# Kernel tuning notes

Measured on AMD Instinct MI355X. Metric: run time of the kernel, lower is better.

## Reference

```python
import jax, jax.numpy as jnp
import numpy as np

N_NODES = 100000
N_EDGES = 1600000
HIDDEN = 128
N_GRAPHS = 64
N_CLASSES = 10


def setup_inputs() -> dict:
    key = jax.random.key(0)
    ks = jax.random.split(key, 10)
    x = jax.random.normal(ks[0], (N_NODES, 1), dtype=jnp.float32)
    edge_index = jax.random.randint(ks[1], (2, N_EDGES), 0, N_NODES, dtype=jnp.int32)
    batch = jnp.sort(jax.random.randint(ks[2], (N_NODES,), 0, N_GRAPHS, dtype=jnp.int32))
    def glorot(k, shape):
        fan_in, fan_out = shape
        s = jnp.sqrt(6.0 / (fan_in + fan_out))
        return jax.random.uniform(k, shape, jnp.float32, -s, s)
    return {
        "x": x,
        "edge_index": edge_index,
        "batch": batch,
        "W1l": glorot(ks[3], (1, HIDDEN)),
        "W1r": glorot(ks[4], (1, HIDDEN)),
        "b1": jnp.zeros((HIDDEN,), jnp.float32),
        "W2l": glorot(ks[5], (HIDDEN, HIDDEN)),
        "W2r": glorot(ks[6], (HIDDEN, HIDDEN)),
        "b2": jnp.zeros((HIDDEN,), jnp.float32),
        "W3l": glorot(ks[7], (HIDDEN, HIDDEN)),
        "W3r": glorot(ks[8], (HIDDEN, HIDDEN)),
        "b3": jnp.zeros((HIDDEN,), jnp.float32),
        "Wfc": glorot(ks[9], (HIDDEN, N_CLASSES)),
        "bfc": jnp.zeros((N_CLASSES,), jnp.float32),
    }


def _sage_conv(x, src, dst, Wl, Wr, b, n_nodes):
    # mean aggregation of source features at destination nodes
    msg = x[src]                                              # [E, d_in]
    agg = jax.ops.segment_sum(msg, dst, num_segments=n_nodes)  # [N, d_in]
    cnt = jax.ops.segment_sum(jnp.ones((src.shape[0], 1), x.dtype), dst,
                              num_segments=n_nodes)            # [N, 1]
    mean = agg / jnp.maximum(cnt, 1.0)
    # PyG SAGEConv: lin_l(mean neighbors) + bias + lin_r(self)
    return mean @ Wl + b + x @ Wr


def reference(x, edge_index, batch, W1l, W1r, b1, W2l, W2r, b2,
              W3l, W3r, b3, Wfc, bfc):
    src, dst = edge_index[0], edge_index[1]
    n = x.shape[0]
    h = jax.nn.relu(_sage_conv(x, src, dst, W1l, W1r, b1, n))
    h = jax.nn.relu(_sage_conv(h, src, dst, W2l, W2r, b2, n))
    h = jax.nn.relu(_sage_conv(h, src, dst, W3l, W3r, b3, n))
    # global_mean_pool over graph ids in `batch`
    pooled = jax.ops.segment_sum(h, batch, num_segments=N_GRAPHS)
    gcnt = jax.ops.segment_sum(jnp.ones((n, 1), h.dtype), batch,
                               num_segments=N_GRAPHS)
    pooled = pooled / jnp.maximum(gcnt, 1.0)
    logits = pooled @ Wfc + bfc
    return jax.nn.log_softmax(logits, axis=1)
```

## Files before the change

kernel.cpp:

```cpp
#include <hip/hip_runtime.h>

typedef unsigned int u32;
typedef unsigned short u16;
typedef short bf16x8 __attribute__((ext_vector_type(8)));
typedef float f32x4 __attribute__((ext_vector_type(4)));
typedef u32 u32x4 __attribute__((ext_vector_type(4)));

#define HBLK 256

__device__ __forceinline__ u16 f2bf(float f) {
  u32 u = __float_as_uint(f);
  u = (u + 0x7FFFu + ((u >> 16) & 1u)) >> 16;
  return (u16)u;
}
__device__ __forceinline__ float bf2f(u32 h) { return __uint_as_float(h << 16); }

__global__ void hist_kernel(const int* __restrict__ dst, int* __restrict__ hist,
                            int E, int nbuk, int chunk) {
  __shared__ int h[1024];
  for (int i = threadIdx.x; i < nbuk; i += 256) h[i] = 0;
  __syncthreads();
  int b0 = blockIdx.x * chunk, b1 = min(b0 + chunk, E);
  for (int e = b0 + threadIdx.x; e < b1; e += 256)
    atomicAdd(&h[dst[e] >> 7], 1);
  __syncthreads();
  for (int i = threadIdx.x; i < nbuk; i += 256)
    hist[i * HBLK + blockIdx.x] = h[i];
}

__global__ void scan_local(const int* __restrict__ in, int* __restrict__ out,
                           int* __restrict__ bsum, int n) {
  __shared__ int s[256];
  int tid = threadIdx.x;
  int i = blockIdx.x * 256 + tid;
  int v = (i < n) ? in[i] : 0;
  s[tid] = v;
  __syncthreads();
  for (int off = 1; off < 256; off <<= 1) {
    int t = (tid >= off) ? s[tid - off] : 0;
    __syncthreads();
    s[tid] += t;
    __syncthreads();
  }
  if (i < n) out[i] = s[tid] - v;
  if (tid == 255) bsum[blockIdx.x] = s[255];
}

__global__ void scan_fix(int* __restrict__ a, const int* __restrict__ bsum, int n) {
  __shared__ int red[256];
  int tid = threadIdx.x, b = blockIdx.x;
  int s = 0;
  for (int k = tid; k < b; k += 256) s += bsum[k];
  red[tid] = s;
  __syncthreads();
  for (int off = 128; off; off >>= 1) {
    if (tid < off) red[tid] += red[tid + off];
    __syncthreads();
  }
  int i = b * 256 + tid;
  if (i < n) a[i] += red[0];
}

__global__ void scatter2_kernel(const int* __restrict__ src, const int* __restrict__ dst,
                                const int* __restrict__ hist_s, u32* __restrict__ part,
                                int E, int nbuk, int chunk) {
  __shared__ int cur[1024];
  for (int i = threadIdx.x; i < nbuk; i += 256)
    cur[i] = hist_s[i * HBLK + blockIdx.x];
  __syncthreads();
  int b0 = blockIdx.x * chunk, b1 = min(b0 + chunk, E);
  for (int e = b0 + threadIdx.x; e < b1; e += 256) {
    int d = dst[e];
    int pos = atomicAdd(&cur[d >> 7], 1);
    part[pos] = (u32)src[e] | ((u32)(d & 127) << 25);
  }
}

__global__ void scatter3_kernel(const u32* __restrict__ part, const int* __restrict__ hist_s,
                                int* __restrict__ roff, int* __restrict__ csr,
                                int E, int nbuk, int n) {
  int b = blockIdx.x;
  int tid = threadIdx.x;
  int base = hist_s[b * HBLK];
  int end = (b + 1 < nbuk) ? hist_s[(b + 1) * HBLK] : E;
  __shared__ int cnt[128];
  __shared__ int s[128];
  __shared__ int cur[128];
  if (tid < 128) cnt[tid] = 0;
  __syncthreads();
  for (int e = base + tid; e < end; e += 256)
    atomicAdd(&cnt[part[e] >> 25], 1);
  __syncthreads();
  if (tid < 128) s[tid] = cnt[tid];
  __syncthreads();
  for (int off = 1; off < 128; off <<= 1) {
    int t = (tid >= off && tid < 128) ? s[tid - off] : 0;
    __syncthreads();
    if (tid < 128) s[tid] += t;
    __syncthreads();
  }
  if (tid < 128) {
    int excl = s[tid] - cnt[tid];
    cur[tid] = base + excl;
    int node = b * 128 + tid;
    if (node < n) roff[node] = base + excl;
  }
  if (b == 0 && tid == 0) roff[n] = E;
  __syncthreads();
  for (int e = base + tid; e < end; e += 256) {
    u32 p = part[e];
    int pos = atomicAdd(&cur[p >> 25], 1);
    csr[pos] = (int)(p & 0x1FFFFFFu);
  }
}

__global__ void meanh1_kernel(const int* __restrict__ csr, const int* __restrict__ roff,
                              const float* __restrict__ x,
                              const float* __restrict__ W1l, const float* __restrict__ W1r,
                              const float* __restrict__ b1, u32* __restrict__ h1, int n) {
  int wave = threadIdx.x >> 6, lane = threadIdx.x & 63;
  int i = blockIdx.x * 4 + wave;
  if (i >= n) return;
  int e0 = roff[i], e1 = roff[i + 1];
  float s = 0.f;
  for (int e = e0 + lane; e < e1; e += 64) s += x[csr[e]];
#pragma unroll
  for (int off = 1; off < 64; off <<= 1) s += __shfl_xor(s, off, 64);
  float m = s / (float)max(e1 - e0, 1);
  float xs = x[i];
  int j0 = lane * 2;
  float v0 = fmaxf(m * W1l[j0] + xs * W1r[j0] + b1[j0], 0.f);
  float v1 = fmaxf(m * W1l[j0 + 1] + xs * W1r[j0 + 1] + b1[j0 + 1], 0.f);
  h1[(size_t)i * 64 + lane] = (u32)f2bf(v0) | ((u32)f2bf(v1) << 16);
}

__global__ void wprep2_kernel(const float* __restrict__ W2l, const float* __restrict__ W2r,
                              const float* __restrict__ W3l, const float* __restrict__ W3r,
                              u16* __restrict__ wt2, u16* __restrict__ wt3,
                              float* __restrict__ pooled, int* __restrict__ gcnt) {
  int idx = blockIdx.x * 256 + threadIdx.x;
  int which = idx >> 15, r = idx & 32767;
  int j = r >> 8, k = r & 255;
  if (which == 0) {
    float v = (k < 128) ? W2l[k * 128 + j] : W2r[(k - 128) * 128 + j];
    wt2[r] = f2bf(v);
  } else {
    float v = (k < 128) ? W3l[k * 128 + j] : W3r[(k - 128) * 128 + j];
    wt3[r] = f2bf(v);
  }
  if (idx < 8192) pooled[idx] = 0.f;
  if (idx < 64) gcnt[idx] = 0;
}

__global__ void agg_kernel(const int* __restrict__ csr, const int* __restrict__ roff,
                           const u32* __restrict__ hin, u32* __restrict__ outv, int n) {
  int wave = threadIdx.x >> 6, lane = threadIdx.x & 63;
  int i = blockIdx.x * 4 + wave;
  if (i >= n) return;
  int grp = lane >> 4, li = lane & 15;
  int e0 = roff[i], e1 = roff[i + 1];
  float a[8] = {};
  int e = e0 + grp;
  for (; e + 12 < e1; e += 16) {
    int s0 = csr[e], s1 = csr[e + 4], s2 = csr[e + 8], s3 = csr[e + 12];
    u32x4 v0 = *(const u32x4*)(hin + (size_t)s0 * 64 + li * 4);
    u32x4 v1 = *(const u32x4*)(hin + (size_t)s1 * 64 + li * 4);
    u32x4 v2 = *(const u32x4*)(hin + (size_t)s2 * 64 + li * 4);
    u32x4 v3 = *(const u32x4*)(hin + (size_t)s3 * 64 + li * 4);
#pragma unroll
    for (int w = 0; w < 4; ++w) {
      a[2 * w]     += bf2f(v0[w] & 0xFFFFu) + bf2f(v1[w] & 0xFFFFu) +
                      bf2f(v2[w] & 0xFFFFu) + bf2f(v3[w] & 0xFFFFu);
      a[2 * w + 1] += bf2f(v0[w] >> 16) + bf2f(v1[w] >> 16) +
                      bf2f(v2[w] >> 16) + bf2f(v3[w] >> 16);
    }
  }
  for (; e + 4 < e1; e += 8) {
    int s0 = csr[e], s1 = csr[e + 4];
    u32x4 v0 = *(const u32x4*)(hin + (size_t)s0 * 64 + li * 4);
    u32x4 v1 = *(const u32x4*)(hin + (size_t)s1 * 64 + li * 4);
#pragma unroll
    for (int w = 0; w < 4; ++w) {
      a[2 * w]     += bf2f(v0[w] & 0xFFFFu) + bf2f(v1[w] & 0xFFFFu);
      a[2 * w + 1] += bf2f(v0[w] >> 16) + bf2f(v1[w] >> 16);
    }
  }
  if (e < e1) {
    int s0 = csr[e];
    u32x4 v0 = *(const u32x4*)(hin + (size_t)s0 * 64 + li * 4);
#pragma unroll
    for (int w = 0; w < 4; ++w) {
      a[2 * w]     += bf2f(v0[w] & 0xFFFFu);
      a[2 * w + 1] += bf2f(v0[w] >> 16);
    }
  }
#pragma unroll
  for (int w = 0; w < 8; ++w) {
    a[w] += __shfl_xor(a[w], 16, 64);
    a[w] += __shfl_xor(a[w], 32, 64);
  }
  if (grp == 0) {
    float inv = 1.f / (float)max(e1 - e0, 1);
    u32x4 o;
#pragma unroll
    for (int w = 0; w < 4; ++w)
      o[w] = (u32)f2bf(a[2 * w] * inv) | ((u32)f2bf(a[2 * w + 1] * inv) << 16);
    *(u32x4*)(outv + (size_t)i * 64 + li * 4) = o;
  }
}

__launch_bounds__(1024)
__global__ void mm_kernel(const u16* Aleft, const u16* Aright,
                          const u16* __restrict__ Wt, const float* __restrict__ bias,
                          u16* Out, int n) {
  __shared__ u16 wlds[32768];
  for (int c = threadIdx.x; c < 4096; c += 1024) {
    int j = c >> 5, ch = c & 31;
    int swz = ch ^ (j & 31);
    *(u32x4*)(&wlds[j * 256 + swz * 8]) = *(const u32x4*)(&Wt[j * 256 + ch * 8]);
  }
  __syncthreads();
  int wave = threadIdx.x >> 6;
  int lane = threadIdx.x & 63;
  int quad = lane >> 4, l16 = lane & 15;
  int row0 = blockIdx.x * 256 + wave * 16;
  int m = row0 + l16;
  int mc = m < n ? m : (n - 1);
  f32x4 acc[8] = {};
  const u16* Ah[2] = {Aleft, Aright};
#pragma unroll
  for (int half = 0; half < 2; ++half) {
    const u16* A = Ah[half] + (size_t)mc * 128;
#pragma unroll
    for (int s = 0; s < 4; ++s) {
      bf16x8 a = *(const bf16x8*)(A + s * 32 + quad * 8);
      int chunk = (half << 4) + (s << 2) + quad;
#pragma unroll
      for (int t = 0; t < 8; ++t) {
        int j = t * 16 + l16;
        int swz = chunk ^ (j & 31);
        bf16x8 b = *(const bf16x8*)(&wlds[j * 256 + swz * 8]);
        acc[t] = __builtin_amdgcn_mfma_f32_16x16x32_bf16(a, b, acc[t], 0, 0, 0);
      }
    }
  }
#pragma unroll
  for (int t = 0; t < 8; ++t) {
    int j = t * 16 + l16;
    float bj = bias[j];
#pragma unroll
    for (int r = 0; r < 4; ++r) {
      int mr = row0 + quad * 4 + r;
      if (mr < n) {
        float v = acc[t][r] + bj;
        Out[(size_t)mr * 128 + j] = f2bf(fmaxf(v, 0.f));
      }
    }
  }
}

#define PB_NODES 256
__global__ void pool_partial(const int* __restrict__ batch, const u32* __restrict__ h3,
                             float* __restrict__ pooled, int* __restrict__ gcnt, int n) {
  int wave = threadIdx.x >> 6, lane = threadIdx.x & 63;
  int start = blockIdx.x * PB_NODES;
  int end = min(start + PB_NODES, n);
  float a0 = 0.f, a1 = 0.f;
  int gcur = -1, cnt = 0;
  for (int i = start + wave; i < end; i += 4) {
    int g = batch[i];
    if (g != gcur) {
      if (gcur >= 0) {
        atomicAdd(&pooled[gcur * 128 + lane * 2], a0);
        atomicAdd(&pooled[gcur * 128 + lane * 2 + 1], a1);
        if (lane == 0) atomicAdd(&gcnt[gcur], cnt);
      }
      gcur = g; a0 = 0.f; a1 = 0.f; cnt = 0;
    }
    u32 v = h3[(size_t)i * 64 + lane];
    a0 += bf2f(v & 0xFFFFu);
    a1 += bf2f(v >> 16);
    cnt++;
  }
  if (gcur >= 0) {
    atomicAdd(&pooled[gcur * 128 + lane * 2], a0);
    atomicAdd(&pooled[gcur * 128 + lane * 2 + 1], a1);
    if (lane == 0) atomicAdd(&gcnt[gcur], cnt);
  }
}

__global__ void head_kernel(const float* __restrict__ pooled, const int* __restrict__ gcnt,
                            const float* __restrict__ Wfc, const float* __restrict__ bfc,
                            float* __restrict__ out) {
  __shared__ float lg[64][10];
  int t = threadIdx.x;
  if (t < 640) {
    int g = t / 10, c = t % 10;
    float inv = 1.f / (float)max(gcnt[g], 1);
    float acc = bfc[c];
    for (int k = 0; k < 128; ++k) acc += pooled[g * 128 + k] * inv * Wfc[k * 10 + c];
    lg[g][c] = acc;
  }
  __syncthreads();
  if (t < 640) {
    int g = t / 10, c = t % 10;
    float mx = -1e30f;
    for (int q = 0; q < 10; ++q) mx = fmaxf(mx, lg[g][q]);
    float se = 0.f;
    for (int q = 0; q < 10; ++q) se += expf(lg[g][q] - mx);
    out[g * 10 + c] = lg[g][c] - mx - logf(se);
  }
}

extern "C" void kernel_launch(void* const* d_in, const int* in_sizes, int n_in,
                              void* d_out, int out_size, void* d_ws, size_t ws_size,
                              hipStream_t stream) {
  const float* x   = (const float*)d_in[0];
  const int* ei    = (const int*)d_in[1];
  const int* batch = (const int*)d_in[2];
  const float* W1l = (const float*)d_in[3];
  const float* W1r = (const float*)d_in[4];
  const float* b1  = (const float*)d_in[5];
  const float* W2l = (const float*)d_in[6];
  const float* W2r = (const float*)d_in[7];
  const float* b2  = (const float*)d_in[8];
  const float* W3l = (const float*)d_in[9];
  const float* W3r = (const float*)d_in[10];
  const float* b3  = (const float*)d_in[11];
  const float* Wfc = (const float*)d_in[12];
  const float* bfc = (const float*)d_in[13];
  float* out = (float*)d_out;
  int N = in_sizes[0];
  int E = in_sizes[1] / 2;
  const int* src = ei;
  const int* dst = ei + E;

  char* p = (char*)d_ws;
  auto alloc = [&](size_t bytes) { void* r = (void*)p; p += (bytes + 255) & ~(size_t)255; return r; };
  int* roff   = (int*)alloc((size_t)(N + 1) * 4);
  int* csr    = (int*)alloc((size_t)E * 4);
  u32* bufA   = (u32*)alloc((size_t)N * 64 * 4);
  u32* bufB   = (u32*)alloc((size_t)N * 64 * 4);
  u16* wt2    = (u16*)alloc(32768 * 2);
  u16* wt3    = (u16*)alloc(32768 * 2);
  float* pooled = (float*)alloc(64 * 128 * 4);
  int* gcnt   = (int*)alloc(64 * 4);
  int* bsum   = (int*)alloc(1024 * 4);

  int nbuk = (N + 127) >> 7;
  int* hist = (int*)bufA;
  u32* part = (u32*)bufB;
  int chunk = (E + HBLK - 1) / HBLK;
  int nH = nbuk * HBLK;
  int nbH = (nH + 255) / 256;

  hist_kernel<<<HBLK, 256, 0, stream>>>(dst, hist, E, nbuk, chunk);
  scan_local<<<nbH, 256, 0, stream>>>(hist, hist, bsum, nH);
  scan_fix<<<nbH, 256, 0, stream>>>(hist, bsum, nH);
  scatter2_kernel<<<HBLK, 256, 0, stream>>>(src, dst, hist, part, E, nbuk, chunk);
  scatter3_kernel<<<nbuk, 256, 0, stream>>>(part, hist, roff, csr, E, nbuk, N);
  wprep2_kernel<<<256, 256, 0, stream>>>(W2l, W2r, W3l, W3r, wt2, wt3, pooled, gcnt);
  meanh1_kernel<<<(N + 3) / 4, 256, 0, stream>>>(csr, roff, x, W1l, W1r, b1, bufA, N);
  agg_kernel<<<(N + 3) / 4, 256, 0, stream>>>(csr, roff, bufA, bufB, N);
  mm_kernel<<<(N + 255) / 256, 1024, 0, stream>>>((const u16*)bufB, (const u16*)bufA, wt2, b2, (u16*)bufB, N);
  agg_kernel<<<(N + 3) / 4, 256, 0, stream>>>(csr, roff, bufB, bufA, N);
  mm_kernel<<<(N + 255) / 256, 1024, 0, stream>>>((const u16*)bufA, (const u16*)bufB, wt3, b3, (u16*)bufA, N);
  pool_partial<<<(N + PB_NODES - 1) / PB_NODES, 256, 0, stream>>>(batch, bufA, pooled, gcnt, N);
  head_kernel<<<1, 640, 0, stream>>>(pooled, gcnt, Wfc, bfc, out);
}
```

Measured before the change: 364.9 us.

## Fuse layer-1 scalar mean into CSR build, shrink mm blocks, pack agg accumulators

Computes the layer-1 neighbor mean of the scalar input inside the CSR scatter kernel with shared-memory float atomics. This replaces the per-node gather kernel with a flat elementwise h1 kernel and removes one pass over the CSR. The matmul kernel moves from 1024-thread blocks over 256 rows to 512-thread blocks over 128 rows, giving more blocks and possibly better occupancy, at the cost of reloading the weights into LDS more often. The aggregation accumulators are regrouped into float2 vectors, which may let the compiler emit packed adds. Float atomics make the layer-1 sum order nondeterministic.

```diff
diff --git a/kernel.cpp b/kernel.cpp
--- a/kernel.cpp
+++ b/kernel.cpp
@@ -4,6 +4,7 @@
 typedef unsigned short u16;
 typedef short bf16x8 __attribute__((ext_vector_type(8)));
 typedef float f32x4 __attribute__((ext_vector_type(4)));
+typedef float f32x2 __attribute__((ext_vector_type(2)));
 typedef u32 u32x4 __attribute__((ext_vector_type(4)));
 
 #define HBLK 256
@@ -77,8 +78,9 @@
 }
 
 __global__ void scatter3_kernel(const u32* __restrict__ part, const int* __restrict__ hist_s,
+                                const float* __restrict__ x,
                                 int* __restrict__ roff, int* __restrict__ csr,
-                                int E, int nbuk, int n) {
+                                float* __restrict__ mean1, int E, int nbuk, int n) {
   int b = blockIdx.x;
   int tid = threadIdx.x;
   int base = hist_s[b * HBLK];
@@ -86,7 +88,8 @@
   __shared__ int cnt[128];
   __shared__ int s[128];
   __shared__ int cur[128];
-  if (tid < 128) cnt[tid] = 0;
+  __shared__ float xsum[128];
+  if (tid < 128) { cnt[tid] = 0; xsum[tid] = 0.f; }
   __syncthreads();
   for (int e = base + tid; e < end; e += 256)
     atomicAdd(&cnt[part[e] >> 25], 1);
@@ -109,29 +112,29 @@
   __syncthreads();
   for (int e = base + tid; e < end; e += 256) {
     u32 p = part[e];
+    int sidx = (int)(p & 0x1FFFFFFu);
     int pos = atomicAdd(&cur[p >> 25], 1);
-    csr[pos] = (int)(p & 0x1FFFFFFu);
-  }
-}
-
-__global__ void meanh1_kernel(const int* __restrict__ csr, const int* __restrict__ roff,
-                              const float* __restrict__ x,
-                              const float* __restrict__ W1l, const float* __restrict__ W1r,
-                              const float* __restrict__ b1, u32* __restrict__ h1, int n) {
-  int wave = threadIdx.x >> 6, lane = threadIdx.x & 63;
-  int i = blockIdx.x * 4 + wave;
-  if (i >= n) return;
-  int e0 = roff[i], e1 = roff[i + 1];
-  float s = 0.f;
-  for (int e = e0 + lane; e < e1; e += 64) s += x[csr[e]];
-#pragma unroll
-  for (int off = 1; off < 64; off <<= 1) s += __shfl_xor(s, off, 64);
-  float m = s / (float)max(e1 - e0, 1);
-  float xs = x[i];
-  int j0 = lane * 2;
-  float v0 = fmaxf(m * W1l[j0] + xs * W1r[j0] + b1[j0], 0.f);
-  float v1 = fmaxf(m * W1l[j0 + 1] + xs * W1r[j0 + 1] + b1[j0 + 1], 0.f);
-  h1[(size_t)i * 64 + lane] = (u32)f2bf(v0) | ((u32)f2bf(v1) << 16);
+    csr[pos] = sidx;
+    atomicAdd(&xsum[p >> 25], x[sidx]);
+  }
+  __syncthreads();
+  if (tid < 128) {
+    int node = b * 128 + tid;
+    if (node < n) mean1[node] = xsum[tid] / (float)max(cnt[tid], 1);
+  }
+}
+
+__global__ void h1_kernel(const float* __restrict__ mean1, const float* __restrict__ x,
+                          const float* __restrict__ W1l, const float* __restrict__ W1r,
+                          const float* __restrict__ b1, u32* __restrict__ h1, int n) {
+  int idx = blockIdx.x * 256 + threadIdx.x;
+  if (idx >= n * 64) return;
+  int i = idx >> 6, w = idx & 63;
+  int j0 = w * 2;
+  float m1 = mean1[i], xs = x[i];
+  float v0 = fmaxf(m1 * W1l[j0] + xs * W1r[j0] + b1[j0], 0.f);
+  float v1 = fmaxf(m1 * W1l[j0 + 1] + xs * W1r[j0 + 1] + b1[j0 + 1], 0.f);
+  h1[idx] = (u32)f2bf(v0) | ((u32)f2bf(v1) << 16);
 }
 
 __global__ void wprep2_kernel(const float* __restrict__ W2l, const float* __restrict__ W2r,
@@ -159,7 +162,7 @@
   if (i >= n) return;
   int grp = lane >> 4, li = lane & 15;
   int e0 = roff[i], e1 = roff[i + 1];
-  float a[8] = {};
+  f32x2 a[4] = {};
   int e = e0 + grp;
   for (; e + 12 < e1; e += 16) {
     int s0 = csr[e], s1 = csr[e + 4], s2 = csr[e + 8], s3 = csr[e + 12];
@@ -169,10 +172,10 @@
     u32x4 v3 = *(const u32x4*)(hin + (size_t)s3 * 64 + li * 4);
 #pragma unroll
     for (int w = 0; w < 4; ++w) {
-      a[2 * w]     += bf2f(v0[w] & 0xFFFFu) + bf2f(v1[w] & 0xFFFFu) +
-                      bf2f(v2[w] & 0xFFFFu) + bf2f(v3[w] & 0xFFFFu);
-      a[2 * w + 1] += bf2f(v0[w] >> 16) + bf2f(v1[w] >> 16) +
-                      bf2f(v2[w] >> 16) + bf2f(v3[w] >> 16);
+      a[w] += (f32x2){bf2f(v0[w] & 0xFFFFu), bf2f(v0[w] >> 16)};
+      a[w] += (f32x2){bf2f(v1[w] & 0xFFFFu), bf2f(v1[w] >> 16)};
+      a[w] += (f32x2){bf2f(v2[w] & 0xFFFFu), bf2f(v2[w] >> 16)};
+      a[w] += (f32x2){bf2f(v3[w] & 0xFFFFu), bf2f(v3[w] >> 16)};
     }
   }
   for (; e + 4 < e1; e += 8) {
@@ -181,40 +184,40 @@
     u32x4 v1 = *(const u32x4*)(hin + (size_t)s1 * 64 + li * 4);
 #pragma unroll
     for (int w = 0; w < 4; ++w) {
-      a[2 * w]     += bf2f(v0[w] & 0xFFFFu) + bf2f(v1[w] & 0xFFFFu);
-      a[2 * w + 1] += bf2f(v0[w] >> 16) + bf2f(v1[w] >> 16);
+      a[w] += (f32x2){bf2f(v0[w] & 0xFFFFu), bf2f(v0[w] >> 16)};
+      a[w] += (f32x2){bf2f(v1[w] & 0xFFFFu), bf2f(v1[w] >> 16)};
     }
   }
   if (e < e1) {
     int s0 = csr[e];
     u32x4 v0 = *(const u32x4*)(hin + (size_t)s0 * 64 + li * 4);
 #pragma unroll
-    for (int w = 0; w < 4; ++w) {
-      a[2 * w]     += bf2f(v0[w] & 0xFFFFu);
-      a[2 * w + 1] += bf2f(v0[w] >> 16);
-    }
-  }
-#pragma unroll
-  for (int w = 0; w < 8; ++w) {
-    a[w] += __shfl_xor(a[w], 16, 64);
-    a[w] += __shfl_xor(a[w], 32, 64);
+    for (int w = 0; w < 4; ++w)
+      a[w] += (f32x2){bf2f(v0[w] & 0xFFFFu), bf2f(v0[w] >> 16)};
+  }
+#pragma unroll
+  for (int w = 0; w < 4; ++w) {
+    a[w].x += __shfl_xor(a[w].x, 16, 64);
+    a[w].y += __shfl_xor(a[w].y, 16, 64);
+    a[w].x += __shfl_xor(a[w].x, 32, 64);
+    a[w].y += __shfl_xor(a[w].y, 32, 64);
   }
   if (grp == 0) {
     float inv = 1.f / (float)max(e1 - e0, 1);
     u32x4 o;
 #pragma unroll
     for (int w = 0; w < 4; ++w)
-      o[w] = (u32)f2bf(a[2 * w] * inv) | ((u32)f2bf(a[2 * w + 1] * inv) << 16);
+      o[w] = (u32)f2bf(a[w].x * inv) | ((u32)f2bf(a[w].y * inv) << 16);
     *(u32x4*)(outv + (size_t)i * 64 + li * 4) = o;
   }
 }
 
-__launch_bounds__(1024)
+__launch_bounds__(512)
 __global__ void mm_kernel(const u16* Aleft, const u16* Aright,
                           const u16* __restrict__ Wt, const float* __restrict__ bias,
                           u16* Out, int n) {
   __shared__ u16 wlds[32768];
-  for (int c = threadIdx.x; c < 4096; c += 1024) {
+  for (int c = threadIdx.x; c < 4096; c += 512) {
     int j = c >> 5, ch = c & 31;
     int swz = ch ^ (j & 31);
     *(u32x4*)(&wlds[j * 256 + swz * 8]) = *(const u32x4*)(&Wt[j * 256 + ch * 8]);
@@ -223,7 +226,7 @@
   int wave = threadIdx.x >> 6;
   int lane = threadIdx.x & 63;
   int quad = lane >> 4, l16 = lane & 15;
-  int row0 = blockIdx.x * 256 + wave * 16;
+  int row0 = blockIdx.x * 128 + wave * 16;
   int m = row0 + l16;
   int mc = m < n ? m : (n - 1);
   f32x4 acc[8] = {};
@@ -339,6 +342,7 @@
   auto alloc = [&](size_t bytes) { void* r = (void*)p; p += (bytes + 255) & ~(size_t)255; return r; };
   int* roff   = (int*)alloc((size_t)(N + 1) * 4);
   int* csr    = (int*)alloc((size_t)E * 4);
+  float* mean1 = (float*)alloc((size_t)N * 4);
   u32* bufA   = (u32*)alloc((size_t)N * 64 * 4);
   u32* bufB   = (u32*)alloc((size_t)N * 64 * 4);
   u16* wt2    = (u16*)alloc(32768 * 2);
@@ -358,13 +362,13 @@
   scan_local<<<nbH, 256, 0, stream>>>(hist, hist, bsum, nH);
   scan_fix<<<nbH, 256, 0, stream>>>(hist, bsum, nH);
   scatter2_kernel<<<HBLK, 256, 0, stream>>>(src, dst, hist, part, E, nbuk, chunk);
-  scatter3_kernel<<<nbuk, 256, 0, stream>>>(part, hist, roff, csr, E, nbuk, N);
+  scatter3_kernel<<<nbuk, 256, 0, stream>>>(part, hist, x, roff, csr, mean1, E, nbuk, N);
   wprep2_kernel<<<256, 256, 0, stream>>>(W2l, W2r, W3l, W3r, wt2, wt3, pooled, gcnt);
-  meanh1_kernel<<<(N + 3) / 4, 256, 0, stream>>>(csr, roff, x, W1l, W1r, b1, bufA, N);
+  h1_kernel<<<((size_t)N * 64 + 255) / 256, 256, 0, stream>>>(mean1, x, W1l, W1r, b1, bufA, N);
   agg_kernel<<<(N + 3) / 4, 256, 0, stream>>>(csr, roff, bufA, bufB, N);
-  mm_kernel<<<(N + 255) / 256, 1024, 0, stream>>>((const u16*)bufB, (const u16*)bufA, wt2, b2, (u16*)bufB, N);
+  mm_kernel<<<(N + 127) / 128, 512, 0, stream>>>((const u16*)bufB, (const u16*)bufA, wt2, b2, (u16*)bufB, N);
   agg_kernel<<<(N + 3) / 4, 256, 0, stream>>>(csr, roff, bufB, bufA, N);
-  mm_kernel<<<(N + 255) / 256, 1024, 0, stream>>>((const u16*)bufA, (const u16*)bufB, wt3, b3, (u16*)bufA, N);
+  mm_kernel<<<(N + 127) / 128, 512, 0, stream>>>((const u16*)bufA, (const u16*)bufB, wt3, b3, (u16*)bufA, N);
   pool_partial<<<(N + PB_NODES - 1) / PB_NODES, 256, 0, stream>>>(batch, bufA, pooled, gcnt, N);
   head_kernel<<<1, 640, 0, stream>>>(pooled, gcnt, Wfc, bfc, out);
 }
```

After: 368.0 us. No clear change (+0.9%).
